# Optimization experiments

Measured on AMD Instinct MI355X. Metric: run time of the kernel, lower is better.

The kernel has to match this reference:

```python
import jax, jax.numpy as jnp
import numpy as np

D_MODEL = 1024
NHEADS = 16
E_HEAD = D_MODEL // NHEADS  # 64
ROPE_BASE = 10000.0


def _rope_cos_sin(L, dim, base, dtype):
    # dim = E_head (even); inv_freq over pairs, GPT-NeoX half-split convention
    inv_freq = 1.0 / (base ** (jnp.arange(0, dim, 2, dtype=jnp.float32) / dim))
    pos = jnp.arange(L, dtype=jnp.float32)
    freqs = pos[:, None] * inv_freq[None, :]  # [L, dim/2]
    return jnp.cos(freqs).astype(dtype), jnp.sin(freqs).astype(dtype)


def _apply_rope(t, cos, sin):
    # t: [B, H, L, Dh]; rotate-half formulation
    d2 = t.shape[-1] // 2
    t1, t2 = t[..., :d2], t[..., d2:]
    return jnp.concatenate([t1 * cos - t2 * sin, t1 * sin + t2 * cos], axis=-1)


def setup_inputs() -> dict:
    key = jax.random.key(0)
    ks = jax.random.split(key, 5)
    B, L = 4, 2048
    x = jax.random.normal(ks[0], (B, L, D_MODEL), dtype=jnp.float32)
    s_in = 1.0 / np.sqrt(D_MODEL)
    W_packed = jax.random.normal(ks[1], (3 * D_MODEL, D_MODEL), dtype=jnp.float32) * s_in
    b_packed = jax.random.normal(ks[2], (3 * D_MODEL,), dtype=jnp.float32) * 0.02
    W_out = jax.random.normal(ks[3], (D_MODEL, D_MODEL), dtype=jnp.float32) * s_in
    b_out = jax.random.normal(ks[4], (D_MODEL,), dtype=jnp.float32) * 0.02
    return {"x": x, "W_packed": W_packed, "b_packed": b_packed, "W_out": W_out, "b_out": b_out}


def reference(x, W_packed, b_packed, W_out, b_out):
    B, L, _ = x.shape
    # 1) packed QKV projection (query is key is value path)
    qkv = jnp.einsum('ble,fe->blf', x, W_packed) + b_packed  # [B, L, 3*D]
    q, k, v = jnp.split(qkv, 3, axis=-1)
    # 2) split heads -> [B, H, L, Dh]
    def heads(t):
        return t.reshape(B, L, NHEADS, E_HEAD).transpose(0, 2, 1, 3)
    q, k, v = heads(q), heads(k), heads(v)
    # 3) RoPE on q, k
    cos, sin = _rope_cos_sin(L, E_HEAD, ROPE_BASE, x.dtype)
    q = _apply_rope(q, cos, sin)
    k = _apply_rope(k, cos, sin)
    # 4) SDPA (non-causal, no dropout)
    scale = 1.0 / np.sqrt(E_HEAD)
    scores = jnp.einsum('bhqd,bhkd->bhqk', q, k) * scale
    attn = jax.nn.softmax(scores, axis=-1)
    out = jnp.einsum('bhqk,bhkd->bhqd', attn, v)
    # 5) merge heads + output projection
    out = out.transpose(0, 2, 1, 3).reshape(B, L, D_MODEL)
    return jnp.einsum('bld,ed->ble', out, W_out) + b_out
```

## Files before the change

kernel.cpp:

```cpp
#include <hip/hip_runtime.h>
#include <hip/hip_bf16.h>
#include <stdint.h>

#define L_SEQ 2048
#define NB    4
#define NH    16
#define EH    64
#define DM    1024
#define MTOT  (NB * L_SEQ)

typedef __attribute__((ext_vector_type(8))) short bf16x8;
typedef __attribute__((ext_vector_type(4))) float f32x4;
typedef __attribute__((ext_vector_type(16))) float f32x16;

static __device__ __forceinline__ float bf2f(short u) {
    union { unsigned int i; float f; } c;
    c.i = ((unsigned int)(unsigned short)u) << 16;
    return c.f;
}
static __device__ __forceinline__ short f2bf(float f) {
    union { float f; unsigned int i; } c; c.f = f;
    unsigned int x = c.i;
    unsigned int r = (x + 0x7fffu + ((x >> 16) & 1u)) >> 16;
    return (short)(unsigned short)r;
}
static __device__ __forceinline__ unsigned cvtpk(float lo, float hi) {
    unsigned r;
    asm volatile("v_cvt_pk_bf16_f32 %0, %1, %2" : "=v"(r) : "v"(lo), "v"(hi));
    return r;
}

static __device__ __forceinline__ void gload_lds16(const void* g, void* lds) {
    __builtin_amdgcn_global_load_lds(
        (const __attribute__((address_space(1))) unsigned int*)g,
        (__attribute__((address_space(3))) unsigned int*)lds, 16, 0, 0);
}

__global__ __launch_bounds__(256) void cvt3_k(const float* __restrict__ x,
                                              const float* __restrict__ wp,
                                              const float* __restrict__ wo,
                                              short* __restrict__ xb,
                                              short* __restrict__ wpb,
                                              short* __restrict__ wob,
                                              float* __restrict__ tab) {
    int bid = blockIdx.x;
    if (bid >= 12288) {
        int i = (bid - 12288) * 256 + threadIdx.x;
        int l = i >> 5, d = i & 31;
        float inv = powf(10000.0f, -(float)d * (1.0f / 32.0f));
        float fr = (float)l * inv;
        tab[i]         = cosf(fr);
        tab[65536 + i] = sinf(fr);
        return;
    }
    const float* src; short* dst; int i;
    if (bid < 8192)       { src = x;  dst = xb;  i = bid * 256 + threadIdx.x; }
    else if (bid < 11264) { src = wp; dst = wpb; i = (bid - 8192) * 256 + threadIdx.x; }
    else                  { src = wo; dst = wob; i = (bid - 11264) * 256 + threadIdx.x; }
    float4 v = ((const float4*)src)[i];
    short4 o;
    o.x = f2bf(v.x); o.y = f2bf(v.y); o.z = f2bf(v.z); o.w = f2bf(v.w);
    ((short4*)dst)[i] = o;
}

template<int OUTBF16, int NBN, int NCOL, int EPI>
__global__ __launch_bounds__(512, 2) void gemmA_k(const short* __restrict__ A,
                                                  const short* __restrict__ Bt,
                                                  const float* __restrict__ bias,
                                                  void* __restrict__ Cv,
                                                  short* __restrict__ Qp,
                                                  short* __restrict__ Kp,
                                                  short* __restrict__ Vt,
                                                  const float* __restrict__ tab) {
    __shared__ short lds[3][384 * 32];
    const int t = threadIdx.x;
    const int w = t >> 6, l = t & 63;
    const int wm = w >> 1, wn = w & 1;
    const int lr = l & 15, lh = l >> 4;

    const int nblk = NBN * 32;
    int fid = blockIdx.x + blockIdx.y * NBN;
    int swz = (fid & 7) * (nblk >> 3) + (fid >> 3);
    const int n0 = (swz % NBN) * 128;
    const int m0 = (swz / NBN) * 256;

    const int lrow = l >> 2;
    const int schunk = (l & 3) ^ ((l >> 3) & 3);

    const short* Ag = A + (size_t)(m0 + lrow) * 1024 + schunk * 8;
    const short* Bg = Bt + (size_t)(n0 + lrow) * 1024 + schunk * 8;

    auto STAGE = [&](int kt, short* dst) {
        gload_lds16(Ag + (size_t)(w * 32) * 1024 + kt * 32,      dst + (w * 32) * 32);
        gload_lds16(Ag + (size_t)(w * 32 + 16) * 1024 + kt * 32, dst + (w * 32 + 16) * 32);
        gload_lds16(Bg + (size_t)(w * 16) * 1024 + kt * 32,      dst + 8192 + (w * 16) * 32);
    };

    f32x4 acc[4][4] = {};

    STAGE(0, &lds[0][0]);
    STAGE(1, &lds[1][0]);
    asm volatile("s_waitcnt vmcnt(3)" ::: "memory");
    __builtin_amdgcn_s_barrier();

    short* Pc = &lds[0][0];
    short* Pn = &lds[1][0];
    short* Pf = &lds[2][0];

    const int fch = (lh ^ ((lr >> 1) & 3)) << 3;

    for (int kt = 0; kt < 32; ++kt) {
        if (kt < 30) STAGE(kt + 2, Pf);

        const short* Al = Pc;
        const short* Bl = Pc + 8192;

        bf16x8 bfr[4], af[4];
#pragma unroll
        for (int nj = 0; nj < 4; ++nj)
            bfr[nj] = *(const bf16x8*)(Bl + (wn * 64 + nj * 16 + lr) * 32 + fch);
#pragma unroll
        for (int mi = 0; mi < 4; ++mi)
            af[mi] = *(const bf16x8*)(Al + (wm * 64 + mi * 16 + lr) * 32 + fch);

        __builtin_amdgcn_s_setprio(1);
#pragma unroll
        for (int mi = 0; mi < 4; ++mi)
#pragma unroll
            for (int nj = 0; nj < 4; ++nj)
                acc[mi][nj] = __builtin_amdgcn_mfma_f32_16x16x32_bf16(
                    af[mi], bfr[nj], acc[mi][nj], 0, 0, 0);
        __builtin_amdgcn_s_setprio(0);

        asm volatile("s_waitcnt lgkmcnt(0)" ::: "memory");
        if (kt < 30) asm volatile("s_waitcnt vmcnt(3)" ::: "memory");
        else         asm volatile("s_waitcnt vmcnt(0)" ::: "memory");
        __builtin_amdgcn_s_barrier();

        short* tp = Pc; Pc = Pn; Pn = Pf; Pf = tp;
    }

    if (EPI == 0) {
#pragma unroll
        for (int mi = 0; mi < 4; ++mi) {
#pragma unroll
            for (int nj = 0; nj < 4; ++nj) {
                const int row = m0 + wm * 64 + mi * 16 + lh * 4;
                const int col = n0 + wn * 64 + nj * 16 + lr;
                const float bsv = bias[col];
#pragma unroll
                for (int j = 0; j < 4; ++j) {
                    float v = acc[mi][nj][j] + bsv;
                    if (OUTBF16)
                        ((short*)Cv)[(size_t)(row + j) * NCOL + col] = f2bf(v);
                    else
                        ((float*)Cv)[(size_t)(row + j) * NCOL + col] = v;
                }
            }
        }
    } else {
        const int part = n0 >> 10;
        const int h = ((n0 & 1023) >> 6) + wn;
        if (part == 2) {
#pragma unroll
            for (int mi = 0; mi < 4; ++mi) {
                const int r0 = m0 + wm * 64 + mi * 16 + lh * 4;
                const int bq = r0 >> 11, lq = r0 & 2047;
                const int lpb = (lq & ~63) + (((mi * 2 + (lh & 1)) ^ (lr & 7)) << 3) + ((lh >> 1) * 4);
#pragma unroll
                for (int nj = 0; nj < 4; ++nj) {
                    const int d = nj * 16 + lr;
                    const float bsv = bias[n0 + wn * 64 + d];
                    short4 sv;
                    sv.x = f2bf(acc[mi][nj][0] + bsv);
                    sv.y = f2bf(acc[mi][nj][1] + bsv);
                    sv.z = f2bf(acc[mi][nj][2] + bsv);
                    sv.w = f2bf(acc[mi][nj][3] + bsv);
                    *(short4*)(Vt + (size_t)((bq * 16 + h) * 64 + d) * 2048 + lpb) = sv;
                }
            }
        } else {
            const float qsc = (part == 0) ? 0.18033688011112042f : 1.0f;
            short* Dst = (part == 0) ? Qp : Kp;
            const float b1l = bias[n0 + wn * 64 + lr];
            const float b1h = bias[n0 + wn * 64 + 16 + lr];
            const float b2l = bias[n0 + wn * 64 + 32 + lr];
            const float b2h = bias[n0 + wn * 64 + 48 + lr];
#pragma unroll
            for (int mi = 0; mi < 4; ++mi) {
                const int r0 = m0 + wm * 64 + mi * 16 + lh * 4;
                const int bq = r0 >> 11, lq0 = r0 & 2047;
                short* Drow = Dst + ((size_t)(bq * 16 + h) * 2048 + lq0) * 64;
#pragma unroll
                for (int j = 0; j < 4; ++j) {
                    const int ll = lq0 + j;
                    const int r7l = ll & 7;
#pragma unroll
                    for (int njl = 0; njl < 2; ++njl) {
                        const int d2 = njl * 16 + lr;
                        const float c = tab[ll * 32 + d2];
                        const float s = tab[65536 + ll * 32 + d2];
                        const float t1 = acc[mi][njl][j]     + (njl ? b1h : b1l);
                        const float t2 = acc[mi][njl + 2][j] + (njl ? b2h : b2l);
                        const float e1 = (t1 * c - t2 * s) * qsc;
                        const float e2 = (t1 * s + t2 * c) * qsc;
                        if (part == 0) {
                            Drow[j * 64 + d2]      = f2bf(e1);
                            Drow[j * 64 + d2 + 32] = f2bf(e2);
                        } else {
                            Drow[j * 64 + (((d2 >> 3) ^ r7l) * 8) + (d2 & 7)]       = f2bf(e1);
                            Drow[j * 64 + ((((d2 >> 3) | 4) ^ r7l) * 8) + (d2 & 7)] = f2bf(e2);
                        }
                    }
                }
            }
        }
    }
}

__global__ __launch_bounds__(512, 2) void attn_k(const short* __restrict__ Qg,
                                                 const short* __restrict__ Kg,
                                                 const short* __restrict__ Vt,
                                                 short* __restrict__ O) {
    __shared__ short Ks[3][64 * 64];
    __shared__ short Vs[3][64 * 64];
    const int t = threadIdx.x;
    const int w = t >> 6, l = t & 63;
    const int q = l & 31, hi = l >> 5;
    const int r7 = l & 7;

    const int od = blockIdx.x + blockIdx.y * 8;
    const int qblk = (od >> 3) & 7;
    const int bh = (od & 7) * 8 + (od >> 6);
    const int q0 = qblk * 256;

    const short* Qb = Qg + (size_t)bh * (2048 * 64);
    const short* Kb = Kg + (size_t)bh * (2048 * 64);
    const short* Vb = Vt + (size_t)bh * (64 * 2048);

    const int qrow = q0 + w * 32 + q;
    bf16x8 qf[4];
#pragma unroll
    for (int ds = 0; ds < 4; ds++)
        qf[ds] = *(const bf16x8*)(Qb + (size_t)qrow * 64 + ds * 16 + hi * 8);

    const short one_bf = (short)0x3F80;
    const bf16x8 ones = {one_bf, one_bf, one_bf, one_bf, one_bf, one_bf, one_bf, one_bf};

    f32x16 o0 = {}, o1 = {}, os = {};

    const int grow = w * 8 + (l >> 3);
    const int gcol = r7 * 8;

    gload_lds16(Kb + (size_t)grow * 64 + gcol,        &Ks[0][w * 512]);
    gload_lds16(Vb + (size_t)grow * 2048 + gcol,      &Vs[0][w * 512]);
    gload_lds16(Kb + (size_t)(64 + grow) * 64 + gcol, &Ks[1][w * 512]);
    gload_lds16(Vb + (size_t)grow * 2048 + 64 + gcol, &Vs[1][w * 512]);
    asm volatile("s_waitcnt vmcnt(2)" ::: "memory");
    __builtin_amdgcn_s_barrier();

    const short* Kc = &Ks[0][0];  const short* Vc = &Vs[0][0];
    const short* Kn = &Ks[1][0];  const short* Vn = &Vs[1][0];
    short*       Kf = &Ks[2][0];  short*       Vf = &Vs[2][0];

    for (int it = 0; it < 32; ++it) {
        if (it < 30) {
            const int kn = (it + 2) * 64;
            gload_lds16(Kb + (size_t)(kn + grow) * 64 + gcol, Kf + w * 512);
            gload_lds16(Vb + (size_t)grow * 2048 + kn + gcol, Vf + w * 512);
        }

        f32x16 s0 = {}, s1 = {};
#pragma unroll
        for (int ds = 0; ds < 4; ds++) {
            const int ch = ((ds << 1) | hi) ^ r7;
            bf16x8 k0f = *(const bf16x8*)(Kc + q * 64 + ch * 8);
            bf16x8 k1f = *(const bf16x8*)(Kc + (32 + q) * 64 + ch * 8);
            __builtin_amdgcn_s_setprio(1);
            s0 = __builtin_amdgcn_mfma_f32_32x32x16_bf16(k0f, qf[ds], s0, 0, 0, 0);
            s1 = __builtin_amdgcn_mfma_f32_32x32x16_bf16(k1f, qf[ds], s1, 0, 0, 0);
            __builtin_amdgcn_s_setprio(0);
        }

#pragma unroll
        for (int r = 0; r < 16; r++) {
            s0[r] = __builtin_amdgcn_exp2f(s0[r]);
            s1[r] = __builtin_amdgcn_exp2f(s1[r]);
        }

        bf16x8 pf[4];
        {
            union { unsigned u[4]; bf16x8 v; } f;
            f.u[0] = cvtpk(s0[0], s0[1]);  f.u[1] = cvtpk(s0[2], s0[3]);
            f.u[2] = cvtpk(s0[4], s0[5]);  f.u[3] = cvtpk(s0[6], s0[7]);
            pf[0] = f.v;
            f.u[0] = cvtpk(s0[8], s0[9]);  f.u[1] = cvtpk(s0[10], s0[11]);
            f.u[2] = cvtpk(s0[12], s0[13]); f.u[3] = cvtpk(s0[14], s0[15]);
            pf[1] = f.v;
            f.u[0] = cvtpk(s1[0], s1[1]);  f.u[1] = cvtpk(s1[2], s1[3]);
            f.u[2] = cvtpk(s1[4], s1[5]);  f.u[3] = cvtpk(s1[6], s1[7]);
            pf[2] = f.v;
            f.u[0] = cvtpk(s1[8], s1[9]);  f.u[1] = cvtpk(s1[10], s1[11]);
            f.u[2] = cvtpk(s1[12], s1[13]); f.u[3] = cvtpk(s1[14], s1[15]);
            pf[3] = f.v;
        }

#pragma unroll
        for (int ks = 0; ks < 4; ks++) {
            const int ch = ((ks << 1) | hi) ^ r7;
            bf16x8 v0f = *(const bf16x8*)(Vc + q * 64 + ch * 8);
            bf16x8 v1f = *(const bf16x8*)(Vc + (32 + q) * 64 + ch * 8);
            __builtin_amdgcn_s_setprio(1);
            o0 = __builtin_amdgcn_mfma_f32_32x32x16_bf16(v0f, pf[ks], o0, 0, 0, 0);
            o1 = __builtin_amdgcn_mfma_f32_32x32x16_bf16(v1f, pf[ks], o1, 0, 0, 0);
            os = __builtin_amdgcn_mfma_f32_32x32x16_bf16(ones, pf[ks], os, 0, 0, 0);
            __builtin_amdgcn_s_setprio(0);
        }

        asm volatile("s_waitcnt lgkmcnt(0)" ::: "memory");
        if (it < 30) asm volatile("s_waitcnt vmcnt(2)" ::: "memory");
        else         asm volatile("s_waitcnt vmcnt(0)" ::: "memory");
        __builtin_amdgcn_s_barrier();

        const short* tk = Kc; Kc = Kn; Kn = Kf; Kf = (short*)tk;
        const short* tv = Vc; Vc = Vn; Vn = Vf; Vf = (short*)tv;
    }

    const float inv = 1.0f / os[0];
    const int b = bh >> 4, h = bh & 15;
    short* Orow = O + (size_t)(b * 2048 + qrow) * 1024 + h * 64;
#pragma unroll
    for (int g = 0; g < 4; g++) {
        unsigned w0 = cvtpk(o0[g * 4 + 0] * inv, o0[g * 4 + 1] * inv);
        unsigned w1 = cvtpk(o0[g * 4 + 2] * inv, o0[g * 4 + 3] * inv);
        unsigned long long p0 = (unsigned long long)w0 | ((unsigned long long)w1 << 32);
        *(unsigned long long*)(Orow + g * 8 + hi * 4) = p0;
        unsigned w2 = cvtpk(o1[g * 4 + 0] * inv, o1[g * 4 + 1] * inv);
        unsigned w3 = cvtpk(o1[g * 4 + 2] * inv, o1[g * 4 + 3] * inv);
        unsigned long long p1 = (unsigned long long)w2 | ((unsigned long long)w3 << 32);
        *(unsigned long long*)(Orow + 32 + g * 8 + hi * 4) = p1;
    }
}

extern "C" void kernel_launch(void* const* d_in, const int* in_sizes, int n_in,
                              void* d_out, int out_size, void* d_ws, size_t ws_size,
                              hipStream_t stream) {
    const float* x  = (const float*)d_in[0];
    const float* Wp = (const float*)d_in[1];
    const float* bp = (const float*)d_in[2];
    const float* Wo = (const float*)d_in[3];
    const float* bo = (const float*)d_in[4];

    char* ws = (char*)d_ws;
    const size_t SZ_XB  = (size_t)MTOT * DM * 2;
    const size_t SZ_WPB = (size_t)3 * DM * DM * 2;
    const size_t SZ_WOB = (size_t)DM * DM * 2;
    const size_t SZ_BHLE = (size_t)MTOT * DM * 2;

    short* xb   = (short*)(ws);
    short* wpb  = (short*)(ws + SZ_XB);
    short* wob  = (short*)(ws + SZ_XB + SZ_WPB);
    short* Qb   = (short*)(ws + SZ_XB + SZ_WPB + SZ_WOB);
    short* Kb   = (short*)(ws + SZ_XB + SZ_WPB + SZ_WOB + SZ_BHLE);
    short* Vtb  = (short*)(ws + SZ_XB + SZ_WPB + SZ_WOB + 2 * SZ_BHLE);
    short* Ob   = (short*)(ws + SZ_XB + SZ_WPB + SZ_WOB + 3 * SZ_BHLE);
    float* tab  = (float*)(ws + SZ_XB + SZ_WPB + SZ_WOB + 4 * SZ_BHLE);

    cvt3_k<<<12544, 256, 0, stream>>>(x, Wp, Wo, xb, wpb, wob, tab);

    gemmA_k<1, 24, 3072, 1><<<dim3(24, 32), 512, 0, stream>>>(
        xb, wpb, bp, nullptr, Qb, Kb, Vtb, tab);

    attn_k<<<dim3(8, 64), 512, 0, stream>>>(Qb, Kb, Vtb, Ob);

    gemmA_k<0, 8, 1024, 0><<<dim3(8, 32), 512, 0, stream>>>(
        Ob, wob, bo, (float*)d_out, nullptr, nullptr, nullptr, nullptr);
}
```

Before: 180.6 us.

## Software-pipeline QK^T of next tile with PV of current tile; drop ones-MFMA rowsum

Restructures the attention loop so the QK^T MFMAs for the next key tile interleave with the PV MFMAs of the current tile. The first score tile is computed in a prologue before the loop. The row sum now comes from fp32 VALU adds plus a permlane32 swap instead of a third MFMA against a ones vector, which removes a quarter of the PV-phase MFMA work. Launch bounds are raised to 4 waves per EU, which tightens the register budget and risks spills. The vmcnt waits are retuned to the new load ordering.

Result: faster. 176.8 us (median of 3 runs) (-2.1%).

```diff
diff --git a/kernel.cpp b/kernel.cpp
--- a/kernel.cpp
+++ b/kernel.cpp
@@ -12,6 +12,7 @@
 typedef __attribute__((ext_vector_type(8))) short bf16x8;
 typedef __attribute__((ext_vector_type(4))) float f32x4;
 typedef __attribute__((ext_vector_type(16))) float f32x16;
+typedef __attribute__((ext_vector_type(2))) unsigned uint2v;
 
 static __device__ __forceinline__ float bf2f(short u) {
     union { unsigned int i; float f; } c;
@@ -28,6 +29,12 @@
     unsigned r;
     asm volatile("v_cvt_pk_bf16_f32 %0, %1, %2" : "=v"(r) : "v"(lo), "v"(hi));
     return r;
+}
+static __device__ __forceinline__ float pairsum(float x) {
+    union { float f; unsigned u; } c; c.f = x;
+    uint2v r = __builtin_amdgcn_permlane32_swap(c.u, c.u, false, false);
+    union { unsigned u; float f; } a, b; a.u = r[0]; b.u = r[1];
+    return a.f + b.f;
 }
 
 static __device__ __forceinline__ void gload_lds16(const void* g, void* lds) {
@@ -218,7 +225,7 @@
     }
 }
 
-__global__ __launch_bounds__(512, 2) void attn_k(const short* __restrict__ Qg,
+__global__ __launch_bounds__(512, 4) void attn_k(const short* __restrict__ Qg,
                                                  const short* __restrict__ Kg,
                                                  const short* __restrict__ Vt,
                                                  short* __restrict__ O) {
@@ -238,17 +245,6 @@
     const short* Kb = Kg + (size_t)bh * (2048 * 64);
     const short* Vb = Vt + (size_t)bh * (64 * 2048);
 
-    const int qrow = q0 + w * 32 + q;
-    bf16x8 qf[4];
-#pragma unroll
-    for (int ds = 0; ds < 4; ds++)
-        qf[ds] = *(const bf16x8*)(Qb + (size_t)qrow * 64 + ds * 16 + hi * 8);
-
-    const short one_bf = (short)0x3F80;
-    const bf16x8 ones = {one_bf, one_bf, one_bf, one_bf, one_bf, one_bf, one_bf, one_bf};
-
-    f32x16 o0 = {}, o1 = {}, os = {};
-
     const int grow = w * 8 + (l >> 3);
     const int gcol = r7 * 8;
 
@@ -256,7 +252,59 @@
     gload_lds16(Vb + (size_t)grow * 2048 + gcol,      &Vs[0][w * 512]);
     gload_lds16(Kb + (size_t)(64 + grow) * 64 + gcol, &Ks[1][w * 512]);
     gload_lds16(Vb + (size_t)grow * 2048 + 64 + gcol, &Vs[1][w * 512]);
-    asm volatile("s_waitcnt vmcnt(2)" ::: "memory");
+
+    const int qrow = q0 + w * 32 + q;
+    bf16x8 qf[4];
+#pragma unroll
+    for (int ds = 0; ds < 4; ds++)
+        qf[ds] = *(const bf16x8*)(Qb + (size_t)qrow * 64 + ds * 16 + hi * 8);
+
+    f32x16 o0 = {}, o1 = {};
+    float lsumT = 0.0f;
+    bf16x8 pf[4];
+
+    asm volatile("s_waitcnt vmcnt(3)" ::: "memory");
+    __builtin_amdgcn_s_barrier();
+
+    {
+        f32x16 s0 = {}, s1 = {};
+#pragma unroll
+        for (int ds = 0; ds < 4; ds++) {
+            const int ch = ((ds << 1) | hi) ^ r7;
+            bf16x8 k0f = *(const bf16x8*)(&Ks[0][0] + q * 64 + ch * 8);
+            bf16x8 k1f = *(const bf16x8*)(&Ks[0][0] + (32 + q) * 64 + ch * 8);
+            s0 = __builtin_amdgcn_mfma_f32_32x32x16_bf16(k0f, qf[ds], s0, 0, 0, 0);
+            s1 = __builtin_amdgcn_mfma_f32_32x32x16_bf16(k1f, qf[ds], s1, 0, 0, 0);
+        }
+#pragma unroll
+        for (int r = 0; r < 16; r++) {
+            s0[r] = __builtin_amdgcn_exp2f(s0[r]);
+            s1[r] = __builtin_amdgcn_exp2f(s1[r]);
+        }
+        float ts[16];
+#pragma unroll
+        for (int r = 0; r < 16; r++) ts[r] = s0[r] + s1[r];
+#pragma unroll
+        for (int st = 8; st >= 1; st >>= 1)
+#pragma unroll
+            for (int i = 0; i < 8; i++) if (i < st) ts[i] = ts[i] + ts[i + st];
+        lsumT += pairsum(ts[0]);
+        union { unsigned u[4]; bf16x8 v; } f;
+        f.u[0] = cvtpk(s0[0], s0[1]);  f.u[1] = cvtpk(s0[2], s0[3]);
+        f.u[2] = cvtpk(s0[4], s0[5]);  f.u[3] = cvtpk(s0[6], s0[7]);
+        pf[0] = f.v;
+        f.u[0] = cvtpk(s0[8], s0[9]);  f.u[1] = cvtpk(s0[10], s0[11]);
+        f.u[2] = cvtpk(s0[12], s0[13]); f.u[3] = cvtpk(s0[14], s0[15]);
+        pf[1] = f.v;
+        f.u[0] = cvtpk(s1[0], s1[1]);  f.u[1] = cvtpk(s1[2], s1[3]);
+        f.u[2] = cvtpk(s1[4], s1[5]);  f.u[3] = cvtpk(s1[6], s1[7]);
+        pf[2] = f.v;
+        f.u[0] = cvtpk(s1[8], s1[9]);  f.u[1] = cvtpk(s1[10], s1[11]);
+        f.u[2] = cvtpk(s1[12], s1[13]); f.u[3] = cvtpk(s1[14], s1[15]);
+        pf[3] = f.v;
+    }
+
+    asm volatile("s_waitcnt vmcnt(1)" ::: "memory");
     __builtin_amdgcn_s_barrier();
 
     const short* Kc = &Ks[0][0];  const short* Vc = &Vs[0][0];
@@ -272,24 +320,38 @@
 
         f32x16 s0 = {}, s1 = {};
 #pragma unroll
-        for (int ds = 0; ds < 4; ds++) {
-            const int ch = ((ds << 1) | hi) ^ r7;
-            bf16x8 k0f = *(const bf16x8*)(Kc + q * 64 + ch * 8);
-            bf16x8 k1f = *(const bf16x8*)(Kc + (32 + q) * 64 + ch * 8);
+        for (int ks = 0; ks < 4; ks++) {
+            const int ch = ((ks << 1) | hi) ^ r7;
+            bf16x8 v0f = *(const bf16x8*)(Vc + q * 64 + ch * 8);
+            bf16x8 v1f = *(const bf16x8*)(Vc + (32 + q) * 64 + ch * 8);
             __builtin_amdgcn_s_setprio(1);
-            s0 = __builtin_amdgcn_mfma_f32_32x32x16_bf16(k0f, qf[ds], s0, 0, 0, 0);
-            s1 = __builtin_amdgcn_mfma_f32_32x32x16_bf16(k1f, qf[ds], s1, 0, 0, 0);
+            o0 = __builtin_amdgcn_mfma_f32_32x32x16_bf16(v0f, pf[ks], o0, 0, 0, 0);
+            o1 = __builtin_amdgcn_mfma_f32_32x32x16_bf16(v1f, pf[ks], o1, 0, 0, 0);
             __builtin_amdgcn_s_setprio(0);
-        }
-
-#pragma unroll
-        for (int r = 0; r < 16; r++) {
-            s0[r] = __builtin_amdgcn_exp2f(s0[r]);
-            s1[r] = __builtin_amdgcn_exp2f(s1[r]);
-        }
-
-        bf16x8 pf[4];
-        {
+            if (it < 31) {
+                bf16x8 k0f = *(const bf16x8*)(Kn + q * 64 + ch * 8);
+                bf16x8 k1f = *(const bf16x8*)(Kn + (32 + q) * 64 + ch * 8);
+                __builtin_amdgcn_s_setprio(1);
+                s0 = __builtin_amdgcn_mfma_f32_32x32x16_bf16(k0f, qf[ks], s0, 0, 0, 0);
+                s1 = __builtin_amdgcn_mfma_f32_32x32x16_bf16(k1f, qf[ks], s1, 0, 0, 0);
+                __builtin_amdgcn_s_setprio(0);
+            }
+        }
+
+        if (it < 31) {
+#pragma unroll
+            for (int r = 0; r < 16; r++) {
+                s0[r] = __builtin_amdgcn_exp2f(s0[r]);
+                s1[r] = __builtin_amdgcn_exp2f(s1[r]);
+            }
+            float ts[16];
+#pragma unroll
+            for (int r = 0; r < 16; r++) ts[r] = s0[r] + s1[r];
+#pragma unroll
+            for (int st = 8; st >= 1; st >>= 1)
+#pragma unroll
+                for (int i = 0; i < 8; i++) if (i < st) ts[i] = ts[i] + ts[i + st];
+            lsumT += pairsum(ts[0]);
             union { unsigned u[4]; bf16x8 v; } f;
             f.u[0] = cvtpk(s0[0], s0[1]);  f.u[1] = cvtpk(s0[2], s0[3]);
             f.u[2] = cvtpk(s0[4], s0[5]);  f.u[3] = cvtpk(s0[6], s0[7]);
@@ -305,20 +367,8 @@
             pf[3] = f.v;
         }
 
-#pragma unroll
-        for (int ks = 0; ks < 4; ks++) {
-            const int ch = ((ks << 1) | hi) ^ r7;
-            bf16x8 v0f = *(const bf16x8*)(Vc + q * 64 + ch * 8);
-            bf16x8 v1f = *(const bf16x8*)(Vc + (32 + q) * 64 + ch * 8);
-            __builtin_amdgcn_s_setprio(1);
-            o0 = __builtin_amdgcn_mfma_f32_32x32x16_bf16(v0f, pf[ks], o0, 0, 0, 0);
-            o1 = __builtin_amdgcn_mfma_f32_32x32x16_bf16(v1f, pf[ks], o1, 0, 0, 0);
-            os = __builtin_amdgcn_mfma_f32_32x32x16_bf16(ones, pf[ks], os, 0, 0, 0);
-            __builtin_amdgcn_s_setprio(0);
-        }
-
         asm volatile("s_waitcnt lgkmcnt(0)" ::: "memory");
-        if (it < 30) asm volatile("s_waitcnt vmcnt(2)" ::: "memory");
+        if (it < 30) asm volatile("s_waitcnt vmcnt(1)" ::: "memory");
         else         asm volatile("s_waitcnt vmcnt(0)" ::: "memory");
         __builtin_amdgcn_s_barrier();
 
@@ -326,7 +376,7 @@
         const short* tv = Vc; Vc = Vn; Vn = Vf; Vf = (short*)tv;
     }
 
-    const float inv = 1.0f / os[0];
+    const float inv = 1.0f / lsumT;
     const int b = bh >> 4, h = bh & 15;
     short* Orow = O + (size_t)(b * 2048 + qrow) * 1024 + h * 64;
 #pragma unroll
```
